# Kernel optimization log

Hardware: AMD Instinct MI355X
Metric: run time of the kernel (lower is better)

## Reference

```python
import jax, jax.numpy as jnp
import numpy as np

N_GRID = 64          # voxels per side (must be 2**i)
SIDE = 2.0           # cube side length, centered at origin (0,0,0)
N1 = N_GRID + 1      # grid points per side
B = 262144           # number of query points
W_FEAT = 256         # feature channels per grid point


def setup_inputs() -> dict:
    key = jax.random.key(0)
    k1, k2, k3 = jax.random.split(key, 3)
    x = jax.random.uniform(k1, (B, 3), minval=-1.0, maxval=1.0, dtype=jnp.float32)
    grid_value = jax.random.normal(k2, (N1 ** 3, 1), dtype=jnp.float32)
    grid_feature = jax.random.normal(k3, (N1 ** 3, W_FEAT), dtype=jnp.float32)
    return {"x": x, "grid_value": grid_value, "grid_feature": grid_feature}


def _trilinear(x, grid_value, grid_feature):
    # Map points into voxel coordinates. Volume is [-SIDE/2, SIDE/2]^3.
    min_c = -SIDE / 2.0
    rel = (x - min_c) * (N_GRID / SIDE)             # (B,3) in [0, N_GRID] if inside
    valid = jnp.all((rel >= 0.0) & (rel <= float(N_GRID)), axis=-1)  # (B,)
    idx = jnp.clip(jnp.floor(rel).astype(jnp.int32), 0, N_GRID - 1)  # (B,3) voxel idx
    t = rel - idx.astype(rel.dtype)                 # (B,3) fractional offset in voxel
    base = (idx[:, 0] * N1 + idx[:, 1]) * N1 + idx[:, 2]            # flat grid-pt idx

    out = jnp.zeros((x.shape[0], 1), x.dtype)
    feat = jnp.zeros((x.shape[0], grid_feature.shape[1]), x.dtype)
    # Fixed 8-corner loop (structural, not over data dims): trilinear gather + weighted sum.
    for ox in (0, 1):
        wx = t[:, 0] if ox else 1.0 - t[:, 0]
        for oy in (0, 1):
            wy = t[:, 1] if oy else 1.0 - t[:, 1]
            for oz in (0, 1):
                wz = t[:, 2] if oz else 1.0 - t[:, 2]
                w = (wx * wy * wz)[:, None]          # (B,1)
                flat = base + (ox * N1 + oy) * N1 + oz
                out = out + w * grid_value[flat]
                feat = feat + w * grid_feature[flat]
    m = valid[:, None]
    # Points outside the volume get 0 (matches out[valid_idx] = ... on a zero tensor).
    return jnp.where(m, out, 0.0), jnp.where(m, feat, 0.0)


def reference(x, grid_value, grid_feature):
    return _trilinear(x, grid_value, grid_feature)
```

## Files before the change

### kernel.cpp

```cpp
#include <hip/hip_runtime.h>

#define NG    64
#define N1i   65
#define BPTS  262144
#define NBUCK 4096
#define CPAD  16

typedef float v4f __attribute__((ext_vector_type(4)));

__device__ __forceinline__ int point_bucket(const float* __restrict__ x, int p) {
    const float rx = (x[3 * p + 0] + 1.0f) * 32.0f;
    const float ry = (x[3 * p + 1] + 1.0f) * 32.0f;
    const float rz = (x[3 * p + 2] + 1.0f) * 32.0f;
    int ix = min(max((int)floorf(rx), 0), NG - 1) >> 2;
    int iy = min(max((int)floorf(ry), 0), NG - 1) >> 2;
    int iz = min(max((int)floorf(rz), 0), NG - 1) >> 2;
    int m = 0;
#pragma unroll
    for (int i = 0; i < 4; ++i) {
        m |= ((ix >> i) & 1) << (3 * i + 2);
        m |= ((iy >> i) & 1) << (3 * i + 1);
        m |= ((iz >> i) & 1) << (3 * i + 0);
    }
    return m;
}

__global__ __launch_bounds__(256) void hist_kernel(
    const float* __restrict__ x, int* __restrict__ table)
{
    const int p = blockIdx.x * 256 + threadIdx.x;
    atomicAdd(&table[point_bucket(x, p) * CPAD], 1);
}

__global__ __launch_bounds__(1024) void scan_kernel(int* __restrict__ table)
{
    __shared__ int sm[1024];
    const int t = threadIdx.x;
    const int c0 = table[(t * 4 + 0) * CPAD], c1 = table[(t * 4 + 1) * CPAD];
    const int c2 = table[(t * 4 + 2) * CPAD], c3 = table[(t * 4 + 3) * CPAD];
    const int s = c0 + c1 + c2 + c3;
    sm[t] = s;
    __syncthreads();
    int val = s;
    for (int off = 1; off < 1024; off <<= 1) {
        const int v = (t >= off) ? sm[t - off] : 0;
        __syncthreads();
        val += v;
        sm[t] = val;
        __syncthreads();
    }
    const int base = val - s;
    table[(t * 4 + 0) * CPAD + 1] = base;
    table[(t * 4 + 1) * CPAD + 1] = base + c0;
    table[(t * 4 + 2) * CPAD + 1] = base + c0 + c1;
    table[(t * 4 + 3) * CPAD + 1] = base + c0 + c1 + c2;
}

__global__ __launch_bounds__(256) void scatter_kernel(
    const float* __restrict__ x, int* __restrict__ table, int* __restrict__ perm)
{
    const int p = blockIdx.x * 256 + threadIdx.x;
    const int pos = atomicAdd(&table[point_bucket(x, p) * CPAD + 1], 1);
    perm[pos] = p;
}

__global__ __launch_bounds__(256) void trilerp_kernel(
    const float*  __restrict__ x,
    const float*  __restrict__ gv,
    const float4* __restrict__ gf,
    const int*    __restrict__ perm,
    float*        __restrict__ outv,
    float4*       __restrict__ outf)
{
    const int lane = threadIdx.x & 63;
    const int bid  = blockIdx.x;
    const int swz  = (bid & 7) * (BPTS / 4 / 8) + (bid >> 3);
    const int slot = swz * 4 + (threadIdx.x >> 6);
    const int p    = perm[slot];

    const float px = x[3 * p + 0];
    const float py = x[3 * p + 1];
    const float pz = x[3 * p + 2];

    const float rx = (px + 1.0f) * 32.0f;
    const float ry = (py + 1.0f) * 32.0f;
    const float rz = (pz + 1.0f) * 32.0f;

    const bool valid = (rx >= 0.0f) & (rx <= 64.0f) &
                       (ry >= 0.0f) & (ry <= 64.0f) &
                       (rz >= 0.0f) & (rz <= 64.0f);

    int ix = (int)floorf(rx); ix = min(max(ix, 0), NG - 1);
    int iy = (int)floorf(ry); iy = min(max(iy, 0), NG - 1);
    int iz = (int)floorf(rz); iz = min(max(iz, 0), NG - 1);

    const float tx = rx - (float)ix;
    const float ty = ry - (float)iy;
    const float tz = rz - (float)iz;

    const int base = (ix * N1i + iy) * N1i + iz;

    const float wx0 = 1.0f - tx, wy0 = 1.0f - ty, wz0 = 1.0f - tz;
    float w[8];
    w[0] = wx0 * wy0 * wz0;
    w[1] = wx0 * wy0 * tz;
    w[2] = wx0 * ty  * wz0;
    w[3] = wx0 * ty  * tz;
    w[4] = tx  * wy0 * wz0;
    w[5] = tx  * wy0 * tz;
    w[6] = tx  * ty  * wz0;
    w[7] = tx  * ty  * tz;

    const int off[8] = {0, 1, N1i, N1i + 1,
                        N1i * N1i, N1i * N1i + 1, N1i * N1i + N1i, N1i * N1i + N1i + 1};

    float4 acc = make_float4(0.f, 0.f, 0.f, 0.f);
#pragma unroll
    for (int c = 0; c < 8; ++c) {
        const float4 v = gf[(size_t)(base + off[c]) * 64 + lane];
        acc.x += w[c] * v.x;
        acc.y += w[c] * v.y;
        acc.z += w[c] * v.z;
        acc.w += w[c] * v.w;
    }
    if (!valid) acc = make_float4(0.f, 0.f, 0.f, 0.f);
    v4f av = {acc.x, acc.y, acc.z, acc.w};
    __builtin_nontemporal_store(av, (v4f*)&outf[(size_t)p * 64 + lane]);

    if (lane == 0) {
        float s = 0.0f;
#pragma unroll
        for (int c = 0; c < 8; ++c) s += w[c] * gv[base + off[c]];
        __builtin_nontemporal_store(valid ? s : 0.0f, &outv[p]);
    }
}

extern "C" void kernel_launch(void* const* d_in, const int* in_sizes, int n_in,
                              void* d_out, int out_size, void* d_ws, size_t ws_size,
                              hipStream_t stream) {
    const float*  x  = (const float*)d_in[0];
    const float*  gv = (const float*)d_in[1];
    const float4* gf = (const float4*)d_in[2];

    float*  outv = (float*)d_out;
    float4* outf = (float4*)((float*)d_out + BPTS);

    int* table = (int*)d_ws;
    int* perm  = table + NBUCK * CPAD;

    hipMemsetAsync(table, 0, NBUCK * CPAD * sizeof(int), stream);
    hist_kernel   <<<BPTS / 256, 256,  0, stream>>>(x, table);
    scan_kernel   <<<1,          1024, 0, stream>>>(table);
    scatter_kernel<<<BPTS / 256, 256,  0, stream>>>(x, table, perm);
    trilerp_kernel<<<BPTS / 4,   256,  0, stream>>>(x, gv, gf, perm, outv, outf);
}
```

Before: 584.9 us.

## Stage per-bucket grid features in LDS and use LDS-local histogram sort

The trilinear kernel now runs one 1024-thread block per 4x4x4 voxel bucket. Each block preloads the bucket's 5x5x5 corner features (125x256 floats, about 128KB) and values into shared memory, then loops over that bucket's sorted points, reading corners from LDS instead of global memory. The counting sort is also restructured into per-group shared-memory histograms, a column sum, a scan, per-group row bases and an LDS-atomic scatter, which replaces the global atomics and the memset. The large LDS footprint allows only one block per CU, and bucket sizes vary, so load balance across blocks may be uneven.

```diff
diff --git a/kernel.cpp b/kernel.cpp
--- a/kernel.cpp
+++ b/kernel.cpp
@@ -1,20 +1,20 @@
 #include <hip/hip_runtime.h>
 
-#define NG    64
-#define N1i   65
-#define BPTS  262144
-#define NBUCK 4096
-#define CPAD  16
+#define NG     64
+#define N1i    65
+#define BPTS   262144
+#define NBUCK  4096
+#define NGRP   128
+#define GRPPTS (BPTS / NGRP)
+#define PPT    2
+#define SMEM_VEC (125 * 64)
 
 typedef float v4f __attribute__((ext_vector_type(4)));
 
-__device__ __forceinline__ int point_bucket(const float* __restrict__ x, int p) {
-    const float rx = (x[3 * p + 0] + 1.0f) * 32.0f;
-    const float ry = (x[3 * p + 1] + 1.0f) * 32.0f;
-    const float rz = (x[3 * p + 2] + 1.0f) * 32.0f;
-    int ix = min(max((int)floorf(rx), 0), NG - 1) >> 2;
-    int iy = min(max((int)floorf(ry), 0), NG - 1) >> 2;
-    int iz = min(max((int)floorf(rz), 0), NG - 1) >> 2;
+__device__ __forceinline__ int point_bucket(float px, float py, float pz) {
+    int ix = min(max((int)floorf((px + 1.0f) * 32.0f), 0), NG - 1) >> 2;
+    int iy = min(max((int)floorf((py + 1.0f) * 32.0f), 0), NG - 1) >> 2;
+    int iz = min(max((int)floorf((pz + 1.0f) * 32.0f), 0), NG - 1) >> 2;
     int m = 0;
 #pragma unroll
     for (int i = 0; i < 4; ++i) {
@@ -25,19 +25,41 @@
     return m;
 }
 
-__global__ __launch_bounds__(256) void hist_kernel(
-    const float* __restrict__ x, int* __restrict__ table)
-{
-    const int p = blockIdx.x * 256 + threadIdx.x;
-    atomicAdd(&table[point_bucket(x, p) * CPAD], 1);
-}
-
-__global__ __launch_bounds__(1024) void scan_kernel(int* __restrict__ table)
+__global__ __launch_bounds__(1024) void hist_kernel(
+    const float* __restrict__ x, int* __restrict__ counts2)
+{
+    __shared__ int h[NBUCK];
+    const int t = threadIdx.x, g = blockIdx.x;
+#pragma unroll
+    for (int k = 0; k < 4; ++k) h[t + k * 1024] = 0;
+    __syncthreads();
+#pragma unroll
+    for (int k = 0; k < PPT; ++k) {
+        const int p = g * GRPPTS + k * 1024 + t;
+        atomicAdd(&h[point_bucket(x[3 * p], x[3 * p + 1], x[3 * p + 2])], 1);
+    }
+    __syncthreads();
+#pragma unroll
+    for (int k = 0; k < 4; ++k)
+        counts2[g * NBUCK + t + k * 1024] = h[t + k * 1024];
+}
+
+__global__ __launch_bounds__(256) void colsum_kernel(
+    const int* __restrict__ counts2, int* __restrict__ tot)
+{
+    const int b = blockIdx.x * 256 + threadIdx.x;
+    int s = 0;
+    for (int g = 0; g < NGRP; ++g) s += counts2[g * NBUCK + b];
+    tot[b] = s;
+}
+
+__global__ __launch_bounds__(1024) void scan_kernel(
+    const int* __restrict__ tot, int* __restrict__ base)
 {
     __shared__ int sm[1024];
     const int t = threadIdx.x;
-    const int c0 = table[(t * 4 + 0) * CPAD], c1 = table[(t * 4 + 1) * CPAD];
-    const int c2 = table[(t * 4 + 2) * CPAD], c3 = table[(t * 4 + 3) * CPAD];
+    const int c0 = tot[t * 4 + 0], c1 = tot[t * 4 + 1];
+    const int c2 = tot[t * 4 + 2], c3 = tot[t * 4 + 3];
     const int s = c0 + c1 + c2 + c3;
     sm[t] = s;
     __syncthreads();
@@ -49,89 +71,139 @@
         sm[t] = val;
         __syncthreads();
     }
-    const int base = val - s;
-    table[(t * 4 + 0) * CPAD + 1] = base;
-    table[(t * 4 + 1) * CPAD + 1] = base + c0;
-    table[(t * 4 + 2) * CPAD + 1] = base + c0 + c1;
-    table[(t * 4 + 3) * CPAD + 1] = base + c0 + c1 + c2;
-}
-
-__global__ __launch_bounds__(256) void scatter_kernel(
-    const float* __restrict__ x, int* __restrict__ table, int* __restrict__ perm)
-{
-    const int p = blockIdx.x * 256 + threadIdx.x;
-    const int pos = atomicAdd(&table[point_bucket(x, p) * CPAD + 1], 1);
-    perm[pos] = p;
-}
-
-__global__ __launch_bounds__(256) void trilerp_kernel(
+    const int b0 = val - s;
+    base[t * 4 + 0] = b0;
+    base[t * 4 + 1] = b0 + c0;
+    base[t * 4 + 2] = b0 + c0 + c1;
+    base[t * 4 + 3] = b0 + c0 + c1 + c2;
+    if (t == 1023) base[4096] = val;
+}
+
+__global__ __launch_bounds__(256) void rowbase_kernel(
+    int* __restrict__ counts2, const int* __restrict__ base)
+{
+    const int b = blockIdx.x * 256 + threadIdx.x;
+    int run = base[b];
+    for (int g = 0; g < NGRP; ++g) {
+        const int c = counts2[g * NBUCK + b];
+        counts2[g * NBUCK + b] = run;
+        run += c;
+    }
+}
+
+__global__ __launch_bounds__(1024) void scatter_kernel(
+    const float* __restrict__ x, const int* __restrict__ counts2,
+    int* __restrict__ perm)
+{
+    __shared__ int h[NBUCK];
+    const int t = threadIdx.x, g = blockIdx.x;
+#pragma unroll
+    for (int k = 0; k < 4; ++k)
+        h[t + k * 1024] = counts2[g * NBUCK + t + k * 1024];
+    __syncthreads();
+#pragma unroll
+    for (int k = 0; k < PPT; ++k) {
+        const int p = g * GRPPTS + k * 1024 + t;
+        const int b = point_bucket(x[3 * p], x[3 * p + 1], x[3 * p + 2]);
+        const int pos = atomicAdd(&h[b], 1);
+        perm[pos] = p;
+    }
+}
+
+__global__ __launch_bounds__(1024) void trilerp_kernel(
     const float*  __restrict__ x,
     const float*  __restrict__ gv,
     const float4* __restrict__ gf,
     const int*    __restrict__ perm,
+    const int*    __restrict__ base,
     float*        __restrict__ outv,
     float4*       __restrict__ outf)
 {
-    const int lane = threadIdx.x & 63;
-    const int bid  = blockIdx.x;
-    const int swz  = (bid & 7) * (BPTS / 4 / 8) + (bid >> 3);
-    const int slot = swz * 4 + (threadIdx.x >> 6);
-    const int p    = perm[slot];
-
-    const float px = x[3 * p + 0];
-    const float py = x[3 * p + 1];
-    const float pz = x[3 * p + 2];
-
-    const float rx = (px + 1.0f) * 32.0f;
-    const float ry = (py + 1.0f) * 32.0f;
-    const float rz = (pz + 1.0f) * 32.0f;
-
-    const bool valid = (rx >= 0.0f) & (rx <= 64.0f) &
-                       (ry >= 0.0f) & (ry <= 64.0f) &
-                       (rz >= 0.0f) & (rz <= 64.0f);
-
-    int ix = (int)floorf(rx); ix = min(max(ix, 0), NG - 1);
-    int iy = (int)floorf(ry); iy = min(max(iy, 0), NG - 1);
-    int iz = (int)floorf(rz); iz = min(max(iz, 0), NG - 1);
-
-    const float tx = rx - (float)ix;
-    const float ty = ry - (float)iy;
-    const float tz = rz - (float)iz;
-
-    const int base = (ix * N1i + iy) * N1i + iz;
-
-    const float wx0 = 1.0f - tx, wy0 = 1.0f - ty, wz0 = 1.0f - tz;
-    float w[8];
-    w[0] = wx0 * wy0 * wz0;
-    w[1] = wx0 * wy0 * tz;
-    w[2] = wx0 * ty  * wz0;
-    w[3] = wx0 * ty  * tz;
-    w[4] = tx  * wy0 * wz0;
-    w[5] = tx  * wy0 * tz;
-    w[6] = tx  * ty  * wz0;
-    w[7] = tx  * ty  * tz;
-
-    const int off[8] = {0, 1, N1i, N1i + 1,
-                        N1i * N1i, N1i * N1i + 1, N1i * N1i + N1i, N1i * N1i + N1i + 1};
-
-    float4 acc = make_float4(0.f, 0.f, 0.f, 0.f);
-#pragma unroll
-    for (int c = 0; c < 8; ++c) {
-        const float4 v = gf[(size_t)(base + off[c]) * 64 + lane];
-        acc.x += w[c] * v.x;
-        acc.y += w[c] * v.y;
-        acc.z += w[c] * v.z;
-        acc.w += w[c] * v.w;
-    }
-    if (!valid) acc = make_float4(0.f, 0.f, 0.f, 0.f);
-    v4f av = {acc.x, acc.y, acc.z, acc.w};
-    __builtin_nontemporal_store(av, (v4f*)&outf[(size_t)p * 64 + lane]);
-
-    if (lane == 0) {
+    extern __shared__ float4 smem4[];
+    float* smem_gv = (float*)&smem4[SMEM_VEC];
+
+    const int tid = threadIdx.x;
+    const int bucket = (blockIdx.x & 7) * (NBUCK / 8) + (blockIdx.x >> 3);
+    int bx = 0, by = 0, bz = 0;
+#pragma unroll
+    for (int i = 0; i < 4; ++i) {
+        bx |= ((bucket >> (3 * i + 2)) & 1) << i;
+        by |= ((bucket >> (3 * i + 1)) & 1) << i;
+        bz |= ((bucket >> (3 * i + 0)) & 1) << i;
+    }
+    const int gx0 = bx * 4, gy0 = by * 4, gz0 = bz * 4;
+
+    for (int i = tid; i < SMEM_VEC; i += 1024) {
+        const int c = i >> 6, f = i & 63;
+        const int cz = c % 5, cyx = c / 5;
+        const int cy = cyx % 5, cx = cyx / 5;
+        const int gidx = ((gx0 + cx) * N1i + (gy0 + cy)) * N1i + (gz0 + cz);
+        smem4[i] = gf[(size_t)gidx * 64 + f];
+    }
+    if (tid < 125) {
+        const int cz = tid % 5, cyx = tid / 5;
+        const int cy = cyx % 5, cx = cyx / 5;
+        smem_gv[tid] = gv[((gx0 + cx) * N1i + (gy0 + cy)) * N1i + (gz0 + cz)];
+    }
+    __syncthreads();
+
+    const int lane = tid & 63;
+    const int wid  = tid >> 6;
+    const int s0 = base[bucket], s1 = base[bucket + 1];
+
+    for (int slot = s0 + wid; slot < s1; slot += 16) {
+        const int p = perm[slot];
+
+        const float rx = (x[3 * p + 0] + 1.0f) * 32.0f;
+        const float ry = (x[3 * p + 1] + 1.0f) * 32.0f;
+        const float rz = (x[3 * p + 2] + 1.0f) * 32.0f;
+
+        const bool valid = (rx >= 0.0f) & (rx <= 64.0f) &
+                           (ry >= 0.0f) & (ry <= 64.0f) &
+                           (rz >= 0.0f) & (rz <= 64.0f);
+
+        int ix = min(max((int)floorf(rx), 0), NG - 1);
+        int iy = min(max((int)floorf(ry), 0), NG - 1);
+        int iz = min(max((int)floorf(rz), 0), NG - 1);
+
+        const float tx = rx - (float)ix;
+        const float ty = ry - (float)iy;
+        const float tz = rz - (float)iz;
+
+        const int lx = ix - gx0, ly = iy - gy0, lz = iz - gz0;
+        const int c0 = lx * 25 + ly * 5 + lz;
+
+        const float wx0 = 1.0f - tx, wy0 = 1.0f - ty, wz0 = 1.0f - tz;
+        float w[8];
+        w[0] = wx0 * wy0 * wz0;
+        w[1] = wx0 * wy0 * tz;
+        w[2] = wx0 * ty  * wz0;
+        w[3] = wx0 * ty  * tz;
+        w[4] = tx  * wy0 * wz0;
+        w[5] = tx  * wy0 * tz;
+        w[6] = tx  * ty  * wz0;
+        w[7] = tx  * ty  * tz;
+
+        const int off[8] = {0, 1, 5, 6, 25, 26, 30, 31};
+
+        float4 acc = make_float4(0.f, 0.f, 0.f, 0.f);
+#pragma unroll
+        for (int c = 0; c < 8; ++c) {
+            const float4 v = smem4[(c0 + off[c]) * 64 + lane];
+            acc.x += w[c] * v.x;
+            acc.y += w[c] * v.y;
+            acc.z += w[c] * v.z;
+            acc.w += w[c] * v.w;
+        }
+        if (!valid) acc = make_float4(0.f, 0.f, 0.f, 0.f);
+        v4f av = {acc.x, acc.y, acc.z, acc.w};
+        __builtin_nontemporal_store(av, (v4f*)&outf[(size_t)p * 64 + lane]);
+
         float s = 0.0f;
 #pragma unroll
-        for (int c = 0; c < 8; ++c) s += w[c] * gv[base + off[c]];
-        __builtin_nontemporal_store(valid ? s : 0.0f, &outv[p]);
+        for (int c = 0; c < 8; ++c) s += w[c] * smem_gv[c0 + off[c]];
+        if (lane == 0)
+            __builtin_nontemporal_store(valid ? s : 0.0f, &outv[p]);
     }
 }
 
@@ -145,12 +217,17 @@
     float*  outv = (float*)d_out;
     float4* outf = (float4*)((float*)d_out + BPTS);
 
-    int* table = (int*)d_ws;
-    int* perm  = table + NBUCK * CPAD;
-
-    hipMemsetAsync(table, 0, NBUCK * CPAD * sizeof(int), stream);
-    hist_kernel   <<<BPTS / 256, 256,  0, stream>>>(x, table);
-    scan_kernel   <<<1,          1024, 0, stream>>>(table);
-    scatter_kernel<<<BPTS / 256, 256,  0, stream>>>(x, table, perm);
-    trilerp_kernel<<<BPTS / 4,   256,  0, stream>>>(x, gv, gf, perm, outv, outf);
-}
+    int* counts2 = (int*)d_ws;
+    int* tot     = counts2 + NGRP * NBUCK;
+    int* base    = tot + NBUCK;
+    int* perm    = base + (NBUCK + 1);
+
+    hist_kernel   <<<NGRP, 1024, 0, stream>>>(x, counts2);
+    colsum_kernel <<<NBUCK / 256, 256, 0, stream>>>(counts2, tot);
+    scan_kernel   <<<1, 1024, 0, stream>>>(tot, base);
+    rowbase_kernel<<<NBUCK / 256, 256, 0, stream>>>(counts2, base);
+    scatter_kernel<<<NGRP, 1024, 0, stream>>>(x, counts2, perm);
+
+    const size_t smem_bytes = SMEM_VEC * sizeof(float4) + 128 * sizeof(float);
+    trilerp_kernel<<<NBUCK, 1024, smem_bytes, stream>>>(x, gv, gf, perm, base, outv, outf);
+}
```

After: 538.6 us. -7.9%, faster.
